# Optimization experiments

Hardware: AMD Instinct MI355X
Metric: run time of the kernel (lower is better)

## Reference

```python
import jax, jax.numpy as jnp
import numpy as np

EPS = 1e-6  # torch F.pairwise_distance eps, added to the difference elementwise

B, Z = 8192, 128
N_CLASSES = 62
P = int(N_CLASSES * 1.5)  # 93 proxies


def pdist(a, b):
    """||a_i - b_j + EPS||_2 for all pairs, without a [N,M,Z] intermediate.
    Expansion: ||a-b||^2 + 2*EPS*sum(a-b) + Z*EPS^2."""
    aa = jnp.sum(a * a, axis=-1)[:, None]
    bb = jnp.sum(b * b, axis=-1)[None, :]
    ab = a @ b.T
    eps_term = 2.0 * EPS * (jnp.sum(a, -1)[:, None] - jnp.sum(b, -1)[None, :]) + a.shape[-1] * EPS * EPS
    return jnp.sqrt(jnp.maximum(aa + bb - 2.0 * ab + eps_term, 0.0))


def setup_inputs() -> dict:
    key = jax.random.key(0)
    k0, k1, k2 = jax.random.split(key, 3)
    z = jax.random.normal(k0, (B, Z), dtype=jnp.float32)
    y_idx = jax.random.randint(k1, (B,), 0, N_CLASSES, dtype=jnp.int32)
    proxies = jax.random.uniform(k2, (P, Z), dtype=jnp.float32)  # nn.init.uniform_
    y_map = jnp.arange(N_CLASSES, dtype=jnp.int32)  # y_to_relative_y_train (unique classes)
    return {"z": z, "y_idx": y_idx, "proxies": proxies, "y_map": y_map}


def reference(z, y_idx, proxies, y_map):
    # F.normalize(proxies, p=2, dim=-1) with 1e-12 clamp
    prx = proxies / jnp.maximum(jnp.linalg.norm(proxies, axis=-1, keepdims=True), 1e-12)
    # y_rel[j] = position where y_to_relative_y_train == y_idx[j] (exactly one match)
    y_rel = jnp.argmax(y_map[None, :] == y_idx[:, None], axis=-1)  # [B]

    anchors = np.arange(0, z.shape[0] - 3, 3)  # static anchor indices i
    z_a = z[anchors]                            # [A,Z]

    # nearest proxy to each anchor
    D_prox = pdist(z_a, prx)                    # [A,P]
    prox_p = prx[jnp.argmin(D_prox, axis=-1)]   # [A,Z]

    # distance from chosen proxy to every sample; restrict to suffix j>=i with same class
    D_pz = pdist(prox_p, z)                     # [A,B]
    mask = (np.arange(z.shape[0])[None, :] >= anchors[:, None]) & \
           (y_rel[None, :] == y_rel[anchors][:, None])  # [A,B], row i always has j=i True
    D_pos = jnp.where(mask, D_pz, -jnp.inf)
    j_p = jnp.argmax(D_pos, axis=-1)            # hardest positive index
    D_p = jnp.take_along_axis(D_pos, j_p[:, None], axis=-1)[:, 0]  # [A]

    # distances from hardest positive to all proxies -> NCA denominator
    D_n = pdist(z[j_p], prx)                    # [A,P]
    losses = D_p + jax.nn.logsumexp(-D_n, axis=-1)  # -log(exp(-D_p)/sum exp(-D_n))
    return jnp.mean(losses)
```

## Files before the change

### kernel.cpp

```cpp
#include <hip/hip_runtime.h>
#include <math.h>

#define B_N   8192
#define Z_D   128
#define P_N   93
#define NCLS  62
#define A_N   2730
#define BCAP  256
#define GT_S  96
#define NPART 683
#define TWO_EPS   2e-6f
#define ZEPS2     (128.0f * 1e-6f * 1e-6f)

#define AT_LD(p)      __hip_atomic_load((p), __ATOMIC_RELAXED, __HIP_MEMORY_SCOPE_AGENT)
#define AT_ST(p, v)   __hip_atomic_store((p), (v), __ATOMIC_RELAXED, __HIP_MEMORY_SCOPE_AGENT)
#define AT_ADDU(p, v) __hip_atomic_fetch_add((p), (v), __ATOMIC_RELAXED, __HIP_MEMORY_SCOPE_AGENT)

__device__ __forceinline__ float wave_sum(float v) {
#pragma unroll
  for (int off = 1; off < 64; off <<= 1) v += __shfl_xor(v, off, 64);
  return v;
}
__device__ __forceinline__ float wave_min(float v) {
#pragma unroll
  for (int off = 1; off < 64; off <<= 1) v = fminf(v, __shfl_xor(v, off, 64));
  return v;
}

__global__ __launch_bounds__(512) void kA(
    const float* __restrict__ z, const int* __restrict__ y_idx,
    const float* __restrict__ prox, const int* __restrict__ y_map,
    float* __restrict__ pp, float* __restrict__ sp,
    float* __restrict__ zz, float* __restrict__ sz, float* __restrict__ w,
    int* __restrict__ cnt, int* __restrict__ bkt, float* __restrict__ GT,
    unsigned int* __restrict__ ctr) {
  __shared__ float linv[6];
  __shared__ float pt[6 * Z_D];
  __shared__ int lcnt;
  const int b = blockIdx.x, tid = threadIdx.x;
  const int lane = tid & 63, wv = tid >> 6;

  if (b == 0 && tid < 17) ctr[tid * 32] = 0u;

  if (b < 256) {
    const int jch = b & 15, kt = b >> 4, k0 = kt * 6;
    const int nk = (kt == 15) ? 3 : 6;
    const int j = jch * 512 + tid;
    const float* __restrict__ zrow = z + (size_t)j * Z_D;
    if (wv < nk) {
      const int k = k0 + wv;
      const float a = prox[k * Z_D + lane];
      const float c = prox[k * Z_D + 64 + lane];
      const float s = wave_sum(a + c);
      const float q = wave_sum(a * a + c * c);
      const float inv = 1.0f / fmaxf(sqrtf(q), 1e-12f);
      if (lane == 0) {
        linv[wv] = inv;
        if (jch == 0) { pp[k] = q * inv * inv; sp[k] = s * inv; }
      }
    }
    __syncthreads();
    {
      const int nf = nk * 32;
      const float4* __restrict__ src = (const float4*)(prox + (size_t)k0 * Z_D);
      for (int t = tid; t < nf; t += 512) {
        const float iv = linv[t >> 5];
        const float4 v = src[t];
        ((float4*)pt)[t] = make_float4(v.x * iv, v.y * iv, v.z * iv, v.w * iv);
      }
    }
    __syncthreads();
    if (kt < 15) {
      float a0 = 0, a1 = 0, a2 = 0, a3 = 0, a4 = 0, a5 = 0;
#pragma unroll 8
      for (int i4 = 0; i4 < Z_D; i4 += 4) {
        const float4 zv = *(const float4*)(zrow + i4);
        const int f = i4 >> 2;
        const float4 q0 = ((const float4*)pt)[0 * 32 + f];
        const float4 q1 = ((const float4*)pt)[1 * 32 + f];
        const float4 q2 = ((const float4*)pt)[2 * 32 + f];
        const float4 q3 = ((const float4*)pt)[3 * 32 + f];
        const float4 q4 = ((const float4*)pt)[4 * 32 + f];
        const float4 q5 = ((const float4*)pt)[5 * 32 + f];
        a0 += zv.x * q0.x + zv.y * q0.y + zv.z * q0.z + zv.w * q0.w;
        a1 += zv.x * q1.x + zv.y * q1.y + zv.z * q1.z + zv.w * q1.w;
        a2 += zv.x * q2.x + zv.y * q2.y + zv.z * q2.z + zv.w * q2.w;
        a3 += zv.x * q3.x + zv.y * q3.y + zv.z * q3.z + zv.w * q3.w;
        a4 += zv.x * q4.x + zv.y * q4.y + zv.z * q4.z + zv.w * q4.w;
        a5 += zv.x * q5.x + zv.y * q5.y + zv.z * q5.z + zv.w * q5.w;
      }
      float* g = GT + (size_t)j * GT_S + k0;
      *(float2*)(g + 0) = make_float2(a0, a1);
      *(float2*)(g + 2) = make_float2(a2, a3);
      *(float2*)(g + 4) = make_float2(a4, a5);
    } else {
      float a0 = 0, a1 = 0, a2 = 0, zs = 0, zq = 0;
#pragma unroll 8
      for (int i4 = 0; i4 < Z_D; i4 += 4) {
        const float4 zv = *(const float4*)(zrow + i4);
        const int f = i4 >> 2;
        const float4 q0 = ((const float4*)pt)[0 * 32 + f];
        const float4 q1 = ((const float4*)pt)[1 * 32 + f];
        const float4 q2 = ((const float4*)pt)[2 * 32 + f];
        zs += zv.x + zv.y + zv.z + zv.w;
        zq += zv.x * zv.x + zv.y * zv.y + zv.z * zv.z + zv.w * zv.w;
        a0 += zv.x * q0.x + zv.y * q0.y + zv.z * q0.z + zv.w * q0.w;
        a1 += zv.x * q1.x + zv.y * q1.y + zv.z * q1.z + zv.w * q1.w;
        a2 += zv.x * q2.x + zv.y * q2.y + zv.z * q2.z + zv.w * q2.w;
      }
      float* g = GT + (size_t)j * GT_S + 90;
      *(float2*)(g) = make_float2(a0, a1);
      g[2] = a2;
      zz[j] = zq;
      sz[j] = zs;
      w[j] = zq - TWO_EPS * zs;
    }
  } else {
    const int c = b - 256;
    if (tid == 0) lcnt = 0;
    __syncthreads();
    const int ym = y_map[c];
    for (int j = tid; j < B_N; j += 512) {
      if (y_idx[j] == ym) {
        const int pos = atomicAdd(&lcnt, 1);
        if (pos < BCAP) bkt[c * BCAP + pos] = j;
      }
    }
    __syncthreads();
    if (tid == 0) cnt[c] = min(lcnt, BCAP);
  }
}

__global__ __launch_bounds__(256) void kB2(
    const int* __restrict__ y_idx, const int* __restrict__ y_map,
    const float* __restrict__ pp, const float* __restrict__ sp,
    const float* __restrict__ zz, const float* __restrict__ sz,
    const float* __restrict__ w,
    const int* __restrict__ cnt, const int* __restrict__ bkt,
    const float* __restrict__ GT, float* partial, unsigned int* ctr,
    float* __restrict__ out) {
  __shared__ float lpp[P_N], lsp[P_N];
  __shared__ int lymap[NCLS];
  __shared__ float part[4];
  const int b = blockIdx.x;
  const int tid = threadIdx.x, lane = tid & 63, wv = tid >> 6;
  if (tid < P_N) { lpp[tid] = pp[tid]; lsp[tid] = sp[tid]; }
  if (tid < NCLS) lymap[tid] = y_map[tid];
  __syncthreads();

  const int wid = b * 4 + wv;
  float loss = 0.0f;
  if (wid < A_N) {
    const int i = 3 * wid;
    const int yi = y_idx[i];
    const unsigned long long mm = __ballot(lane < NCLS && lymap[lane] == yi);
    const int cls = __ffsll(mm) - 1;
    const float zzi = zz[i], szi = sz[i];
    const int kB = lane + 64;

    const float* __restrict__ GTi = GT + (size_t)i * GT_S;
    float v1 = fmaxf(zzi + lpp[lane] - 2.0f * GTi[lane] +
                     TWO_EPS * (szi - lsp[lane]) + ZEPS2, 0.0f);
    int i1 = lane;
    if (kB < P_N) {
      const float v2 = fmaxf(zzi + lpp[kB] - 2.0f * GTi[kB] +
                             TWO_EPS * (szi - lsp[kB]) + ZEPS2, 0.0f);
      if (v2 < v1) { v1 = v2; i1 = kB; }
    }
#pragma unroll
    for (int off = 1; off < 64; off <<= 1) {
      const float ov = __shfl_xor(v1, off, 64);
      const int oi = __shfl_xor(i1, off, 64);
      if (ov < v1 || (ov == v1 && oi < i1)) { v1 = ov; i1 = oi; }
    }
    const int p = i1;

    const float cp = lpp[p] + TWO_EPS * lsp[p] + ZEPS2;
    const int n = cnt[cls];
    const int* __restrict__ bk = bkt + cls * BCAP;
    float best = -INFINITY;
    int bestj = 0x7fffffff;
    for (int t = lane; t < n; t += 64) {
      const int jj = bk[t];
      if (jj >= i) {
        const float vv = fmaxf(cp + w[jj] - 2.0f * GT[(size_t)jj * GT_S + p], 0.0f);
        if (vv > best || (vv == best && jj < bestj)) { best = vv; bestj = jj; }
      }
    }
#pragma unroll
    for (int off = 1; off < 64; off <<= 1) {
      const float ov = __shfl_xor(best, off, 64);
      const int oj = __shfl_xor(bestj, off, 64);
      if (ov > best || (ov == best && oj < bestj)) { best = ov; bestj = oj; }
    }
    const float Dp = sqrtf(best);
    const int jp = bestj;

    const float zzj = zz[jp], szj = sz[jp];
    const float* __restrict__ GTj = GT + (size_t)jp * GT_S;
    const float d1 = sqrtf(fmaxf(zzj + lpp[lane] - 2.0f * GTj[lane] +
                                 TWO_EPS * (szj - lsp[lane]) + ZEPS2, 0.0f));
    float d2 = INFINITY;
    if (kB < P_N)
      d2 = sqrtf(fmaxf(zzj + lpp[kB] - 2.0f * GTj[kB] +
                       TWO_EPS * (szj - lsp[kB]) + ZEPS2, 0.0f));
    const float mn = wave_min(fminf(d1, d2));
    float ss = expf(mn - d1) + ((kB < P_N) ? expf(mn - d2) : 0.0f);
    ss = wave_sum(ss);
    loss = Dp - mn + logf(ss);
  }
  if (lane == 0) part[wv] = (wid < A_N) ? loss : 0.0f;
  __syncthreads();

  if (wv == 0) {
    int last = 0;
    if (lane == 0) {
      AT_ST(&partial[b], part[0] + part[1] + part[2] + part[3]);
      __builtin_amdgcn_s_waitcnt(0);
      const int sub = b & 15;
      const unsigned quota = (sub < 11) ? 43u : 42u;
      const unsigned old = AT_ADDU(&ctr[sub * 32], 1u);
      if (old == quota - 1u) {
        const unsigned so = AT_ADDU(&ctr[16 * 32], 1u);
        if (so == 15u) last = 1;
      }
    }
    last = __shfl(last, 0, 64);
    if (last) {
      float s = 0.0f;
#pragma unroll
      for (int r = 0; r < 11; ++r) {
        const int t = lane + r * 64;
        if (t < NPART) s += AT_LD(&partial[t]);
      }
      s = wave_sum(s);
      if (lane == 0) out[0] = s * (1.0f / (float)A_N);
    }
  }
}

extern "C" void kernel_launch(void* const* d_in, const int* in_sizes, int n_in,
                              void* d_out, int out_size, void* d_ws, size_t ws_size,
                              hipStream_t stream) {
  const float* z = (const float*)d_in[0];
  const int* y_idx = (const int*)d_in[1];
  const float* prox = (const float*)d_in[2];
  const int* y_map = (const int*)d_in[3];
  float* out = (float*)d_out;

  char* ws = (char*)d_ws;
  unsigned int* ctr = (unsigned int*)(ws + 0);
  float* pp    = (float*)(ws + 2560);
  float* sp    = (float*)(ws + 3072);
  float* zz    = (float*)(ws + 3584);
  float* sz    = (float*)(ws + 36352);
  float* w     = (float*)(ws + 69120);
  int*   cnt   = (int*)  (ws + 101888);
  int*   bkt   = (int*)  (ws + 102144);
  float* parts = (float*)(ws + 165632);
  float* GT    = (float*)(ws + 168448);

  kA<<<256 + NCLS, 512, 0, stream>>>(z, y_idx, prox, y_map,
                                     pp, sp, zz, sz, w, cnt, bkt, GT, ctr);
  kB2<<<NPART, 256, 0, stream>>>(y_idx, y_map, pp, sp, zz, sz, w,
                                 cnt, bkt, GT, parts, ctr, out);
}
```

Measured before the change: 81.38 us.

## Retile proxy-dot kernel to 12 proxies per block and prefetch bucket entries

kA now gives each block 256 rows and 12 proxies (8 proxy tiles by 32 row chunks) instead of 512 rows and 6 proxies, so every z row is read from global memory fewer times and each float4 load feeds more FMAs. The accumulators become a register array, which raises register pressure. In kB2 the class-bucket indices and w values (up to 4 per lane) are loaded before the nearest-proxy reduction, so their latency overlaps that work. This assumes a bucket never holds more than 256 entries, which BCAP already enforces.

```diff
diff --git a/kernel.cpp b/kernel.cpp
--- a/kernel.cpp
+++ b/kernel.cpp
@@ -12,6 +12,11 @@
 #define TWO_EPS   2e-6f
 #define ZEPS2     (128.0f * 1e-6f * 1e-6f)
 
+#define JCH_N 32
+#define ROWS  256
+#define KT_N  8
+#define NKF   12
+
 #define AT_LD(p)      __hip_atomic_load((p), __ATOMIC_RELAXED, __HIP_MEMORY_SCOPE_AGENT)
 #define AT_ST(p, v)   __hip_atomic_store((p), (v), __ATOMIC_RELAXED, __HIP_MEMORY_SCOPE_AGENT)
 #define AT_ADDU(p, v) __hip_atomic_fetch_add((p), (v), __ATOMIC_RELAXED, __HIP_MEMORY_SCOPE_AGENT)
@@ -27,15 +32,15 @@
   return v;
 }
 
-__global__ __launch_bounds__(512) void kA(
+__global__ __launch_bounds__(256) void kA(
     const float* __restrict__ z, const int* __restrict__ y_idx,
     const float* __restrict__ prox, const int* __restrict__ y_map,
     float* __restrict__ pp, float* __restrict__ sp,
     float* __restrict__ zz, float* __restrict__ sz, float* __restrict__ w,
     int* __restrict__ cnt, int* __restrict__ bkt, float* __restrict__ GT,
     unsigned int* __restrict__ ctr) {
-  __shared__ float linv[6];
-  __shared__ float pt[6 * Z_D];
+  __shared__ float linv[NKF];
+  __shared__ float pt[NKF * Z_D];
   __shared__ int lcnt;
   const int b = blockIdx.x, tid = threadIdx.x;
   const int lane = tid & 63, wv = tid >> 6;
@@ -43,19 +48,19 @@
   if (b == 0 && tid < 17) ctr[tid * 32] = 0u;
 
   if (b < 256) {
-    const int jch = b & 15, kt = b >> 4, k0 = kt * 6;
-    const int nk = (kt == 15) ? 3 : 6;
-    const int j = jch * 512 + tid;
+    const int jch = b & 31, kt = b >> 5, k0 = kt * NKF;
+    const int nk = (kt == KT_N - 1) ? 9 : NKF;
+    const int j = jch * ROWS + tid;
     const float* __restrict__ zrow = z + (size_t)j * Z_D;
-    if (wv < nk) {
-      const int k = k0 + wv;
+    for (int idx = wv; idx < nk; idx += 4) {
+      const int k = k0 + idx;
       const float a = prox[k * Z_D + lane];
       const float c = prox[k * Z_D + 64 + lane];
       const float s = wave_sum(a + c);
       const float q = wave_sum(a * a + c * c);
       const float inv = 1.0f / fmaxf(sqrtf(q), 1e-12f);
       if (lane == 0) {
-        linv[wv] = inv;
+        linv[idx] = inv;
         if (jch == 0) { pp[k] = q * inv * inv; sp[k] = s * inv; }
       }
     }
@@ -63,54 +68,53 @@
     {
       const int nf = nk * 32;
       const float4* __restrict__ src = (const float4*)(prox + (size_t)k0 * Z_D);
-      for (int t = tid; t < nf; t += 512) {
+      for (int t = tid; t < nf; t += 256) {
         const float iv = linv[t >> 5];
         const float4 v = src[t];
         ((float4*)pt)[t] = make_float4(v.x * iv, v.y * iv, v.z * iv, v.w * iv);
       }
     }
     __syncthreads();
-    if (kt < 15) {
-      float a0 = 0, a1 = 0, a2 = 0, a3 = 0, a4 = 0, a5 = 0;
-#pragma unroll 8
+    if (kt < KT_N - 1) {
+      float a[NKF];
+#pragma unroll
+      for (int m = 0; m < NKF; ++m) a[m] = 0.0f;
+#pragma unroll 4
       for (int i4 = 0; i4 < Z_D; i4 += 4) {
         const float4 zv = *(const float4*)(zrow + i4);
         const int f = i4 >> 2;
-        const float4 q0 = ((const float4*)pt)[0 * 32 + f];
-        const float4 q1 = ((const float4*)pt)[1 * 32 + f];
-        const float4 q2 = ((const float4*)pt)[2 * 32 + f];
-        const float4 q3 = ((const float4*)pt)[3 * 32 + f];
-        const float4 q4 = ((const float4*)pt)[4 * 32 + f];
-        const float4 q5 = ((const float4*)pt)[5 * 32 + f];
-        a0 += zv.x * q0.x + zv.y * q0.y + zv.z * q0.z + zv.w * q0.w;
-        a1 += zv.x * q1.x + zv.y * q1.y + zv.z * q1.z + zv.w * q1.w;
-        a2 += zv.x * q2.x + zv.y * q2.y + zv.z * q2.z + zv.w * q2.w;
-        a3 += zv.x * q3.x + zv.y * q3.y + zv.z * q3.z + zv.w * q3.w;
-        a4 += zv.x * q4.x + zv.y * q4.y + zv.z * q4.z + zv.w * q4.w;
-        a5 += zv.x * q5.x + zv.y * q5.y + zv.z * q5.z + zv.w * q5.w;
+#pragma unroll
+        for (int m = 0; m < NKF; ++m) {
+          const float4 q = ((const float4*)pt)[m * 32 + f];
+          a[m] += zv.x * q.x + zv.y * q.y + zv.z * q.z + zv.w * q.w;
+        }
       }
       float* g = GT + (size_t)j * GT_S + k0;
-      *(float2*)(g + 0) = make_float2(a0, a1);
-      *(float2*)(g + 2) = make_float2(a2, a3);
-      *(float2*)(g + 4) = make_float2(a4, a5);
+#pragma unroll
+      for (int m = 0; m < NKF; m += 2)
+        *(float2*)(g + m) = make_float2(a[m], a[m + 1]);
     } else {
-      float a0 = 0, a1 = 0, a2 = 0, zs = 0, zq = 0;
-#pragma unroll 8
+      float a[9];
+#pragma unroll
+      for (int m = 0; m < 9; ++m) a[m] = 0.0f;
+      float zs = 0.0f, zq = 0.0f;
+#pragma unroll 4
       for (int i4 = 0; i4 < Z_D; i4 += 4) {
         const float4 zv = *(const float4*)(zrow + i4);
         const int f = i4 >> 2;
-        const float4 q0 = ((const float4*)pt)[0 * 32 + f];
-        const float4 q1 = ((const float4*)pt)[1 * 32 + f];
-        const float4 q2 = ((const float4*)pt)[2 * 32 + f];
         zs += zv.x + zv.y + zv.z + zv.w;
         zq += zv.x * zv.x + zv.y * zv.y + zv.z * zv.z + zv.w * zv.w;
-        a0 += zv.x * q0.x + zv.y * q0.y + zv.z * q0.z + zv.w * q0.w;
-        a1 += zv.x * q1.x + zv.y * q1.y + zv.z * q1.z + zv.w * q1.w;
-        a2 += zv.x * q2.x + zv.y * q2.y + zv.z * q2.z + zv.w * q2.w;
-      }
-      float* g = GT + (size_t)j * GT_S + 90;
-      *(float2*)(g) = make_float2(a0, a1);
-      g[2] = a2;
+#pragma unroll
+        for (int m = 0; m < 9; ++m) {
+          const float4 q = ((const float4*)pt)[m * 32 + f];
+          a[m] += zv.x * q.x + zv.y * q.y + zv.z * q.z + zv.w * q.w;
+        }
+      }
+      float* g = GT + (size_t)j * GT_S + 84;
+#pragma unroll
+      for (int m = 0; m < 8; m += 2)
+        *(float2*)(g + m) = make_float2(a[m], a[m + 1]);
+      g[8] = a[8];
       zz[j] = zq;
       sz[j] = zs;
       w[j] = zq - TWO_EPS * zs;
@@ -120,7 +124,7 @@
     if (tid == 0) lcnt = 0;
     __syncthreads();
     const int ym = y_map[c];
-    for (int j = tid; j < B_N; j += 512) {
+    for (int j = tid; j < B_N; j += 256) {
       if (y_idx[j] == ym) {
         const int pos = atomicAdd(&lcnt, 1);
         if (pos < BCAP) bkt[c * BCAP + pos] = j;
@@ -158,6 +162,19 @@
     const float zzi = zz[i], szi = sz[i];
     const int kB = lane + 64;
 
+    const int n = cnt[cls];
+    const int* __restrict__ bk = bkt + cls * BCAP;
+    int pjj[4];
+    float pww[4];
+#pragma unroll
+    for (int r = 0; r < 4; ++r) {
+      const int t = lane + (r << 6);
+      pjj[r] = (t < n) ? bk[t] : -1;
+    }
+#pragma unroll
+    for (int r = 0; r < 4; ++r)
+      pww[r] = (pjj[r] >= i) ? w[pjj[r]] : 0.0f;
+
     const float* __restrict__ GTi = GT + (size_t)i * GT_S;
     float v1 = fmaxf(zzi + lpp[lane] - 2.0f * GTi[lane] +
                      TWO_EPS * (szi - lsp[lane]) + ZEPS2, 0.0f);
@@ -176,14 +193,13 @@
     const int p = i1;
 
     const float cp = lpp[p] + TWO_EPS * lsp[p] + ZEPS2;
-    const int n = cnt[cls];
-    const int* __restrict__ bk = bkt + cls * BCAP;
     float best = -INFINITY;
     int bestj = 0x7fffffff;
-    for (int t = lane; t < n; t += 64) {
-      const int jj = bk[t];
+#pragma unroll
+    for (int r = 0; r < 4; ++r) {
+      const int jj = pjj[r];
       if (jj >= i) {
-        const float vv = fmaxf(cp + w[jj] - 2.0f * GT[(size_t)jj * GT_S + p], 0.0f);
+        const float vv = fmaxf(cp + pww[r] - 2.0f * GT[(size_t)jj * GT_S + p], 0.0f);
         if (vv > best || (vv == best && jj < bestj)) { best = vv; bestj = jj; }
       }
     }
@@ -260,7 +276,7 @@
   float* parts = (float*)(ws + 165632);
   float* GT    = (float*)(ws + 168448);
 
-  kA<<<256 + NCLS, 512, 0, stream>>>(z, y_idx, prox, y_map,
+  kA<<<256 + NCLS, 256, 0, stream>>>(z, y_idx, prox, y_map,
                                      pp, sp, zz, sz, w, cnt, bkt, GT, ctr);
   kB2<<<NPART, 256, 0, stream>>>(y_idx, y_map, pp, sp, zz, sz, w,
                                  cnt, bkt, GT, parts, ctr, out);
```

Result: slower. 84.78 us (+4.2%).
